# Optimization experiments

Measured on AMD Instinct MI355X. Metric: run time of the kernel, lower is better.

The kernel has to match this reference:

```python
import jax, jax.numpy as jnp
import numpy as np

B, W, T, D = 64, 32, 4096, 128

def setup_inputs() -> dict:
    key = jax.random.key(0)
    ks = jax.random.split(key, 10)
    s = 1.0 / np.sqrt(D)
    return {
        "x": jax.random.normal(ks[0], (B, W, T), dtype=jnp.float32),
        "enc_w": jax.random.uniform(ks[1], (D, W), jnp.float32, -1/np.sqrt(W), 1/np.sqrt(W)),
        "enc_b": jax.random.uniform(ks[2], (D,), jnp.float32, -1/np.sqrt(W), 1/np.sqrt(W)),
        "w_ih": jax.random.uniform(ks[3], (3 * D, D), jnp.float32, -s, s),
        "w_hh": jax.random.uniform(ks[4], (3 * D, D), jnp.float32, -s, s),
        "b_ih": jax.random.uniform(ks[5], (3 * D,), jnp.float32, -s, s),
        "b_hh": jax.random.uniform(ks[6], (3 * D,), jnp.float32, -s, s),
        "dec_w": jax.random.uniform(ks[7], (1, D), jnp.float32, -s, s),
        "dec_b": jax.random.uniform(ks[8], (1,), jnp.float32, -s, s),
        "scale": jnp.ones((1,), dtype=jnp.float32),
        "noise_eps": jax.random.normal(ks[9], (B, T), dtype=jnp.float32),
    }

def reference(x, enc_w, enc_b, w_ih, w_hh, b_ih, b_hh, dec_w, dec_b, scale, noise_eps):
    # x: [B, W, T] -> src: [T, B, W]
    src = jnp.transpose(x, (2, 0, 1))
    encoded = src @ enc_w.T + enc_b  # [T, B, D] (dropout is identity at inference)

    def gru_step(h, xt):
        gi = xt @ w_ih.T + b_ih  # [B, 3D]
        gh = h @ w_hh.T + b_hh   # [B, 3D]
        i_r, i_z, i_n = jnp.split(gi, 3, axis=-1)
        h_r, h_z, h_n = jnp.split(gh, 3, axis=-1)
        r = jax.nn.sigmoid(i_r + h_r)
        z = jax.nn.sigmoid(i_z + h_z)
        n = jnp.tanh(i_n + r * h_n)
        h_new = (1.0 - z) * n + z * h
        return h_new, h_new

    h0 = jnp.zeros_like(encoded[0])
    _, res = jax.lax.scan(gru_step, h0, encoded)  # res: [T, B, D]

    out = encoded + res
    out = (out @ dec_w.T + dec_b)[..., 0]  # [T, B]
    out = out.T                            # [B, T]
    noise = scale * noise_eps              # scale * randn_like(x[:, -1, :])
    return jax.nn.relu(out + noise)
```

## Files before the change

### kernel.cpp

```cpp
#include <hip/hip_runtime.h>

#define NB 64
#define NW 32
#define NT 4096
#define ND 128

#define GI_DW 516
#define HR_STRIDE 144

typedef __attribute__((ext_vector_type(8))) short short8;
typedef __attribute__((ext_vector_type(4))) float f32x4;

#define BAR_LGKM() asm volatile("s_waitcnt lgkmcnt(0)\n\ts_barrier" ::: "memory")

static __device__ __forceinline__ float sigm_f(float v) {
    float e = __builtin_amdgcn_exp2f(v * -1.4426950408889634f);
    return __builtin_amdgcn_rcpf(1.0f + e);
}
static __device__ __forceinline__ float tanh_f(float v) {
    float e = __builtin_amdgcn_exp2f(v * 2.8853900817779268f);
    return 1.0f - 2.0f * __builtin_amdgcn_rcpf(1.0f + e);
}
static __device__ __forceinline__ unsigned short f2bf(float f) {
    unsigned u = __float_as_uint(f);
    u += 0x7FFFu + ((u >> 16) & 1u);
    return (unsigned short)(u >> 16);
}

__global__ __launch_bounds__(256) void k_xv(
    const float* __restrict__ x, const float* __restrict__ enc_w,
    const float* __restrict__ enc_b, const float* __restrict__ dec_w,
    const float* __restrict__ dec_b, const float* __restrict__ scale,
    const float* __restrict__ noise, float* __restrict__ out)
{
    __shared__ float v_s[NW];
    __shared__ float c2_s;
    const int tid = threadIdx.x;
    if (tid < NW) {
        float s = 0.0f;
        for (int d = 0; d < ND; ++d) s = fmaf(enc_w[d * NW + tid], dec_w[d], s);
        v_s[tid] = s;
    } else if (tid == 64) {
        float s = 0.0f;
        for (int d = 0; d < ND; ++d) s = fmaf(enc_b[d], dec_w[d], s);
        c2_s = s + dec_b[0];
    }
    __syncthreads();
    const int flat = blockIdx.x * 256 + tid;
    const int b = flat >> 12;
    const int t = flat & (NT - 1);
    float acc = c2_s + scale[0] * noise[flat];
    const float* xr = x + (size_t)b * NW * NT + t;
    #pragma unroll
    for (int w = 0; w < NW; ++w) acc = fmaf(xr[(size_t)w * NT], v_s[w], acc);
    out[flat] = acc;
}

__global__ __launch_bounds__(256, 1) void k_gru(
    const float* __restrict__ x, const float* __restrict__ enc_w,
    const float* __restrict__ enc_b, const float* __restrict__ w_ih,
    const float* __restrict__ w_hh, const float* __restrict__ b_ih,
    const float* __restrict__ b_hh, const float* __restrict__ dec_w,
    float* out)
{
    __shared__ alignas(16) float gi_lds[32 * GI_DW];
    __shared__ float encb_s[ND];
    __shared__ alignas(16) unsigned short h_ring[32 * HR_STRIDE];
    __shared__ alignas(16) float xv_lds[NT];
    __shared__ alignas(16) float out_lds[NT];

    const int tid  = threadIdx.x;
    const int b    = blockIdx.x;
    const int wv   = tid >> 6;
    const int lane = tid & 63;
    const int g    = lane >> 4;
    const int c    = lane & 15;
    const int hi   = g & 1;
    const int d0   = wv * 32 + c;
    const int d1   = d0 + 16;
    const int dl   = wv * 32 + (lane & 31);

    const size_t xbase = (size_t)b * NW * NT;
    float* outb = out + (size_t)b * NT;
    float* encw_s = gi_lds;

    for (int i = tid; i < ND * NW; i += 256) encw_s[i] = enc_w[i];
    if (tid < ND) encb_s[tid] = enc_b[tid];
    for (int i = tid; i < 32 * HR_STRIDE; i += 256) h_ring[i] = 0;
    for (int i = tid; i < NT / 4; i += 256)
        ((float4*)xv_lds)[i] = ((const float4*)outb)[i];
    __syncthreads();

    short8 BR0[4], BZ0[4], BN0[4], BR1[4], BZ1[4], BN1[4];
    #pragma unroll
    for (int kt = 0; kt < 4; ++kt) {
        const float* pr0 = w_hh + (size_t)(0*ND + d0) * ND + kt*32 + g*8;
        const float* pz0 = w_hh + (size_t)(1*ND + d0) * ND + kt*32 + g*8;
        const float* pn0 = w_hh + (size_t)(2*ND + d0) * ND + kt*32 + g*8;
        const float* pr1 = w_hh + (size_t)(0*ND + d1) * ND + kt*32 + g*8;
        const float* pz1 = w_hh + (size_t)(1*ND + d1) * ND + kt*32 + g*8;
        const float* pn1 = w_hh + (size_t)(2*ND + d1) * ND + kt*32 + g*8;
        #pragma unroll
        for (int i = 0; i < 8; ++i) {
            BR0[kt][i] = (short)f2bf(pr0[i]);
            BZ0[kt][i] = (short)f2bf(pz0[i]);
            BN0[kt][i] = (short)f2bf(pn0[i]);
            BR1[kt][i] = (short)f2bf(pr1[i]);
            BZ1[kt][i] = (short)f2bf(pz1[i]);
            BN1[kt][i] = (short)f2bf(pn1[i]);
        }
    }

    short8 BD[4];
    #pragma unroll
    for (int kt = 0; kt < 4; ++kt)
        #pragma unroll
        for (int i = 0; i < 8; ++i)
            BD[kt][i] = (short)f2bf(dec_w[kt*32 + g*8 + i]);

    short8 XR0, XZ0, XN0, XR1, XZ1, XN1;
    {
        const float* rr0 = w_ih + (size_t)(0*ND + d0) * ND;
        const float* rz0 = w_ih + (size_t)(1*ND + d0) * ND;
        const float* rn0 = w_ih + (size_t)(2*ND + d0) * ND;
        const float* rr1 = w_ih + (size_t)(0*ND + d1) * ND;
        const float* rz1 = w_ih + (size_t)(1*ND + d1) * ND;
        const float* rn1 = w_ih + (size_t)(2*ND + d1) * ND;
        #pragma unroll
        for (int i = 0; i < 8; ++i) {
            int w = g*8 + i;
            float ar0 = 0.f, az0 = 0.f, an0 = 0.f, ar1 = 0.f, az1 = 0.f, an1 = 0.f;
            for (int dp = 0; dp < ND; ++dp) {
                float ew = encw_s[dp*NW + w];
                ar0 = fmaf(ew, rr0[dp], ar0);
                az0 = fmaf(ew, rz0[dp], az0);
                an0 = fmaf(ew, rn0[dp], an0);
                ar1 = fmaf(ew, rr1[dp], ar1);
                az1 = fmaf(ew, rz1[dp], az1);
                an1 = fmaf(ew, rn1[dp], an1);
            }
            XR0[i] = (short)f2bf(ar0); XZ0[i] = (short)f2bf(az0); XN0[i] = (short)f2bf(an0);
            XR1[i] = (short)f2bf(ar1); XZ1[i] = (short)f2bf(az1); XN1[i] = (short)f2bf(an1);
        }
    }

    float cR0, cZ0, cGN0, cIN0, cR1, cZ1, cGN1, cIN1;
    {
        const float* rr0 = w_ih + (size_t)(0*ND + d0) * ND;
        const float* rz0 = w_ih + (size_t)(1*ND + d0) * ND;
        const float* rn0 = w_ih + (size_t)(2*ND + d0) * ND;
        const float* rr1 = w_ih + (size_t)(0*ND + d1) * ND;
        const float* rz1 = w_ih + (size_t)(1*ND + d1) * ND;
        const float* rn1 = w_ih + (size_t)(2*ND + d1) * ND;
        float a0 = b_ih[d0], a1 = b_ih[ND+d0], a2 = b_ih[2*ND+d0];
        float e0 = b_ih[d1], e1 = b_ih[ND+d1], e2 = b_ih[2*ND+d1];
        for (int dp = 0; dp < ND; ++dp) {
            float eb = encb_s[dp];
            a0 = fmaf(eb, rr0[dp], a0);
            a1 = fmaf(eb, rz0[dp], a1);
            a2 = fmaf(eb, rn0[dp], a2);
            e0 = fmaf(eb, rr1[dp], e0);
            e1 = fmaf(eb, rz1[dp], e1);
            e2 = fmaf(eb, rn1[dp], e2);
        }
        cR0  = a0 + b_hh[d0];
        cZ0  = a1 + b_hh[ND+d0];
        cGN0 = b_hh[2*ND+d0];
        cIN0 = a2;
        cR1  = e0 + b_hh[d1];
        cZ1  = e1 + b_hh[ND+d1];
        cGN1 = b_hh[2*ND+d1];
        cIN1 = e2;
    }
    const f32x4 cRv0  = {cR0, cR0, cR0, cR0};
    const f32x4 cZv0  = {cZ0, cZ0, cZ0, cZ0};
    const f32x4 cGNv0 = {cGN0, cGN0, cGN0, cGN0};
    const f32x4 cINv0 = {cIN0, cIN0, cIN0, cIN0};
    const f32x4 cRv1  = {cR1, cR1, cR1, cR1};
    const f32x4 cZv1  = {cZ1, cZ1, cZ1, cZ1};
    const f32x4 cGNv1 = {cGN1, cGN1, cGN1, cGN1};
    const f32x4 cINv1 = {cIN1, cIN1, cIN1, cIN1};
    const f32x4 zv    = {0.f, 0.f, 0.f, 0.f};

    __syncthreads();

    float xf[8];
    #pragma unroll
    for (int q = 0; q < 8; ++q)
        xf[q] = x[xbase + (size_t)(g*8 + q) * NT + c];
    {
        short8 xA;
        #pragma unroll
        for (int i = 0; i < 8; ++i) xA[i] = (short)f2bf(xf[i]);
        f32x4 gR0 = __builtin_amdgcn_mfma_f32_16x16x32_bf16(xA, XR0, cRv0, 0, 0, 0);
        f32x4 gZ0 = __builtin_amdgcn_mfma_f32_16x16x32_bf16(xA, XZ0, cZv0, 0, 0, 0);
        f32x4 gN0 = __builtin_amdgcn_mfma_f32_16x16x32_bf16(xA, XN0, cINv0, 0, 0, 0);
        f32x4 gR1 = __builtin_amdgcn_mfma_f32_16x16x32_bf16(xA, XR1, cRv1, 0, 0, 0);
        f32x4 gZ1 = __builtin_amdgcn_mfma_f32_16x16x32_bf16(xA, XZ1, cZv1, 0, 0, 0);
        f32x4 gN1 = __builtin_amdgcn_mfma_f32_16x16x32_bf16(xA, XN1, cINv1, 0, 0, 0);
        #pragma unroll
        for (int r = 0; r < 4; ++r) {
            int ti = 4*g + r;
            f32x4 p0 = {gR0[r], gZ0[r], gN0[r], 0.f};
            f32x4 p1 = {gR1[r], gZ1[r], gN1[r], 0.f};
            *(f32x4*)(gi_lds + (size_t)ti * GI_DW + d0 * 4) = p0;
            *(f32x4*)(gi_lds + (size_t)ti * GI_DW + d1 * 4) = p1;
        }
    }
    #pragma unroll
    for (int q = 0; q < 8; ++q)
        xf[q] = x[xbase + (size_t)(g*8 + q) * NT + 16 + c];

    __syncthreads();

    float h = 0.0f;

    #pragma unroll 1
    for (int t = 0; t < NT; ++t) {
        const short8* hp = (const short8*)(h_ring + (size_t)((t + 31) & 31) * HR_STRIDE);
        const short8 HA0 = hp[0*4 + g];
        const short8 HA1 = hp[1*4 + g];
        const short8 HA2 = hp[2*4 + g];
        const short8 HA3 = hp[3*4 + g];

        const f32x4 giv = *(const f32x4*)(gi_lds + (size_t)(t & 31) * GI_DW + dl * 4);

        f32x4 aR1_0 = __builtin_amdgcn_mfma_f32_16x16x32_bf16(HA0, BR0[0], zv, 0, 0, 0);
        f32x4 aR2_0 = __builtin_amdgcn_mfma_f32_16x16x32_bf16(HA2, BR0[2], zv, 0, 0, 0);
        f32x4 aR1_1 = __builtin_amdgcn_mfma_f32_16x16x32_bf16(HA0, BR1[0], zv, 0, 0, 0);
        f32x4 aR2_1 = __builtin_amdgcn_mfma_f32_16x16x32_bf16(HA2, BR1[2], zv, 0, 0, 0);
        aR1_0 = __builtin_amdgcn_mfma_f32_16x16x32_bf16(HA1, BR0[1], aR1_0, 0, 0, 0);
        aR2_0 = __builtin_amdgcn_mfma_f32_16x16x32_bf16(HA3, BR0[3], aR2_0, 0, 0, 0);
        aR1_1 = __builtin_amdgcn_mfma_f32_16x16x32_bf16(HA1, BR1[1], aR1_1, 0, 0, 0);
        aR2_1 = __builtin_amdgcn_mfma_f32_16x16x32_bf16(HA3, BR1[3], aR2_1, 0, 0, 0);
        f32x4 aZ1_0 = __builtin_amdgcn_mfma_f32_16x16x32_bf16(HA0, BZ0[0], zv, 0, 0, 0);
        f32x4 aZ2_0 = __builtin_amdgcn_mfma_f32_16x16x32_bf16(HA2, BZ0[2], zv, 0, 0, 0);
        f32x4 aZ1_1 = __builtin_amdgcn_mfma_f32_16x16x32_bf16(HA0, BZ1[0], zv, 0, 0, 0);
        f32x4 aZ2_1 = __builtin_amdgcn_mfma_f32_16x16x32_bf16(HA2, BZ1[2], zv, 0, 0, 0);
        aZ1_0 = __builtin_amdgcn_mfma_f32_16x16x32_bf16(HA1, BZ0[1], aZ1_0, 0, 0, 0);
        aZ2_0 = __builtin_amdgcn_mfma_f32_16x16x32_bf16(HA3, BZ0[3], aZ2_0, 0, 0, 0);
        aZ1_1 = __builtin_amdgcn_mfma_f32_16x16x32_bf16(HA1, BZ1[1], aZ1_1, 0, 0, 0);
        aZ2_1 = __builtin_amdgcn_mfma_f32_16x16x32_bf16(HA3, BZ1[3], aZ2_1, 0, 0, 0);
        f32x4 aN1_0 = __builtin_amdgcn_mfma_f32_16x16x32_bf16(HA0, BN0[0], cGNv0, 0, 0, 0);
        f32x4 aN2_0 = __builtin_amdgcn_mfma_f32_16x16x32_bf16(HA2, BN0[2], zv, 0, 0, 0);
        f32x4 aN1_1 = __builtin_amdgcn_mfma_f32_16x16x32_bf16(HA0, BN1[0], cGNv1, 0, 0, 0);
        f32x4 aN2_1 = __builtin_amdgcn_mfma_f32_16x16x32_bf16(HA2, BN1[2], zv, 0, 0, 0);
        aN1_0 = __builtin_amdgcn_mfma_f32_16x16x32_bf16(HA1, BN0[1], aN1_0, 0, 0, 0);
        aN2_0 = __builtin_amdgcn_mfma_f32_16x16x32_bf16(HA3, BN0[3], aN2_0, 0, 0, 0);
        aN1_1 = __builtin_amdgcn_mfma_f32_16x16x32_bf16(HA1, BN1[1], aN1_1, 0, 0, 0);
        aN2_1 = __builtin_amdgcn_mfma_f32_16x16x32_bf16(HA3, BN1[3], aN2_1, 0, 0, 0);

        float R  = hi ? (aR1_1[0] + aR2_1[0]) : (aR1_0[0] + aR2_0[0]);
        float Z  = hi ? (aZ1_1[0] + aZ2_1[0]) : (aZ1_0[0] + aZ2_0[0]);
        float GN = hi ? (aN1_1[0] + aN2_1[0]) : (aN1_0[0] + aN2_0[0]);
        float r_ = sigm_f(R + giv[0]);
        float z_ = sigm_f(Z + giv[1]);
        float n_ = tanh_f(fmaf(r_, GN, giv[2]));
        h = fmaf(z_, h - n_, n_);
        if (lane < 32) h_ring[(size_t)(t & 31) * HR_STRIDE + dl] = f2bf(h);

        if ((t & 15) == 8) {
            const int t0n = (t & ~15) + 16;
            if (t0n < NT) {
                short8 xA;
                #pragma unroll
                for (int i = 0; i < 8; ++i) xA[i] = (short)f2bf(xf[i]);
                f32x4 gR0 = __builtin_amdgcn_mfma_f32_16x16x32_bf16(xA, XR0, cRv0, 0, 0, 0);
                f32x4 gZ0 = __builtin_amdgcn_mfma_f32_16x16x32_bf16(xA, XZ0, cZv0, 0, 0, 0);
                f32x4 gN0 = __builtin_amdgcn_mfma_f32_16x16x32_bf16(xA, XN0, cINv0, 0, 0, 0);
                f32x4 gR1 = __builtin_amdgcn_mfma_f32_16x16x32_bf16(xA, XR1, cRv1, 0, 0, 0);
                f32x4 gZ1 = __builtin_amdgcn_mfma_f32_16x16x32_bf16(xA, XZ1, cZv1, 0, 0, 0);
                f32x4 gN1 = __builtin_amdgcn_mfma_f32_16x16x32_bf16(xA, XN1, cINv1, 0, 0, 0);
                const int rb = t0n & 31;
                #pragma unroll
                for (int r = 0; r < 4; ++r) {
                    int ti = rb + 4*g + r;
                    f32x4 p0 = {gR0[r], gZ0[r], gN0[r], 0.f};
                    f32x4 p1 = {gR1[r], gZ1[r], gN1[r], 0.f};
                    *(f32x4*)(gi_lds + (size_t)ti * GI_DW + d0 * 4) = p0;
                    *(f32x4*)(gi_lds + (size_t)ti * GI_DW + d1 * 4) = p1;
                }
                const int t0p = t0n + 16;
                if (t0p < NT) {
                    #pragma unroll
                    for (int q = 0; q < 8; ++q)
                        xf[q] = x[xbase + (size_t)(g*8 + q) * NT + t0p + c];
                }
            }
        }

        if ((t & 15) == 0 && t >= 16 && wv == (((t >> 4) - 1) & 3)) {
            const short8* hq = (const short8*)(h_ring + (size_t)(((t - 16) & 31) + c) * HR_STRIDE);
            short8 AD0 = hq[0*4 + g];
            short8 AD1 = hq[1*4 + g];
            short8 AD2 = hq[2*4 + g];
            short8 AD3 = hq[3*4 + g];
            f32x4 aD1 = __builtin_amdgcn_mfma_f32_16x16x32_bf16(AD0, BD[0], zv, 0, 0, 0);
            f32x4 aD2 = __builtin_amdgcn_mfma_f32_16x16x32_bf16(AD2, BD[2], zv, 0, 0, 0);
            aD1 = __builtin_amdgcn_mfma_f32_16x16x32_bf16(AD1, BD[1], aD1, 0, 0, 0);
            aD2 = __builtin_amdgcn_mfma_f32_16x16x32_bf16(AD3, BD[3], aD2, 0, 0, 0);
            if (c == 0) {
                #pragma unroll
                for (int r = 0; r < 4; ++r)
                    out_lds[(t - 16) + 4*g + r] = aD1[r] + aD2[r];
            }
        }

        BAR_LGKM();
    }

    if (wv == 0) {
        const short8* hq = (const short8*)(h_ring + (size_t)(16 + c) * HR_STRIDE);
        short8 AD0 = hq[0*4 + g];
        short8 AD1 = hq[1*4 + g];
        short8 AD2 = hq[2*4 + g];
        short8 AD3 = hq[3*4 + g];
        f32x4 aD1 = __builtin_amdgcn_mfma_f32_16x16x32_bf16(AD0, BD[0], zv, 0, 0, 0);
        f32x4 aD2 = __builtin_amdgcn_mfma_f32_16x16x32_bf16(AD2, BD[2], zv, 0, 0, 0);
        aD1 = __builtin_amdgcn_mfma_f32_16x16x32_bf16(AD1, BD[1], aD1, 0, 0, 0);
        aD2 = __builtin_amdgcn_mfma_f32_16x16x32_bf16(AD3, BD[3], aD2, 0, 0, 0);
        if (c == 0) {
            #pragma unroll
            for (int r = 0; r < 4; ++r)
                out_lds[(NT - 16) + 4*g + r] = aD1[r] + aD2[r];
        }
    }
    __syncthreads();
    for (int i = tid; i < NT / 4; i += 256) {
        float4 o = ((const float4*)out_lds)[i];
        float4 v = ((const float4*)xv_lds)[i];
        float4 r;
        r.x = fmaxf(o.x + v.x, 0.0f);
        r.y = fmaxf(o.y + v.y, 0.0f);
        r.z = fmaxf(o.z + v.z, 0.0f);
        r.w = fmaxf(o.w + v.w, 0.0f);
        ((float4*)outb)[i] = r;
    }
}

extern "C" void kernel_launch(void* const* d_in, const int* in_sizes, int n_in,
                              void* d_out, int out_size, void* d_ws, size_t ws_size,
                              hipStream_t stream) {
    const float* x      = (const float*)d_in[0];
    const float* enc_w  = (const float*)d_in[1];
    const float* enc_b  = (const float*)d_in[2];
    const float* w_ih   = (const float*)d_in[3];
    const float* w_hh   = (const float*)d_in[4];
    const float* b_ih   = (const float*)d_in[5];
    const float* b_hh   = (const float*)d_in[6];
    const float* dec_w  = (const float*)d_in[7];
    const float* dec_b  = (const float*)d_in[8];
    const float* scale  = (const float*)d_in[9];
    const float* noise  = (const float*)d_in[10];
    float* out = (float*)d_out;

    k_xv<<<(NB * NT) / 256, 256, 0, stream>>>(x, enc_w, enc_b, dec_w, dec_b, scale, noise, out);
    k_gru<<<NB, 256, 0, stream>>>(x, enc_w, enc_b, w_ih, w_hh, b_ih, b_hh, dec_w, out);
}
```

Baseline: 1.764 ms.

## Specialize waves: recurrence waves separate from input-projection and decoder waves

```diff
diff --git a/kernel.cpp b/kernel.cpp
--- a/kernel.cpp
+++ b/kernel.cpp
@@ -25,6 +25,11 @@
     unsigned u = __float_as_uint(f);
     u += 0x7FFFu + ((u >> 16) & 1u);
     return (unsigned short)(u >> 16);
+}
+static __device__ __forceinline__ unsigned cvt_pk_bf16(float a, float b) {
+    unsigned r;
+    asm("v_cvt_pk_bf16_f32 %0, %1, %2" : "=v"(r) : "v"(a), "v"(b));
+    return r;
 }
 
 __global__ __launch_bounds__(256) void k_xv(
@@ -56,7 +61,7 @@
     out[flat] = acc;
 }
 
-__global__ __launch_bounds__(256, 1) void k_gru(
+__global__ __launch_bounds__(512, 1) void k_gru(
     const float* __restrict__ x, const float* __restrict__ enc_w,
     const float* __restrict__ enc_b, const float* __restrict__ w_ih,
     const float* __restrict__ w_hh, const float* __restrict__ b_ih,
@@ -76,50 +81,55 @@
     const int g    = lane >> 4;
     const int c    = lane & 15;
     const int hi   = g & 1;
-    const int d0   = wv * 32 + c;
+    const int p    = wv - 4;
+    const int dg   = (wv < 4 ? wv : p);
+    const int d0   = dg * 32 + c;
     const int d1   = d0 + 16;
-    const int dl   = wv * 32 + (lane & 31);
+    const int dl   = dg * 32 + (lane & 31);
 
     const size_t xbase = (size_t)b * NW * NT;
     float* outb = out + (size_t)b * NT;
     float* encw_s = gi_lds;
 
-    for (int i = tid; i < ND * NW; i += 256) encw_s[i] = enc_w[i];
+    for (int i = tid; i < ND * NW; i += 512) encw_s[i] = enc_w[i];
     if (tid < ND) encb_s[tid] = enc_b[tid];
-    for (int i = tid; i < 32 * HR_STRIDE; i += 256) h_ring[i] = 0;
-    for (int i = tid; i < NT / 4; i += 256)
+    for (int i = tid; i < 32 * HR_STRIDE; i += 512) h_ring[i] = 0;
+    for (int i = tid; i < NT / 4; i += 512) {
         ((float4*)xv_lds)[i] = ((const float4*)outb)[i];
+        ((float4*)out_lds)[i] = make_float4(0.f, 0.f, 0.f, 0.f);
+    }
     __syncthreads();
 
     short8 BR0[4], BZ0[4], BN0[4], BR1[4], BZ1[4], BN1[4];
-    #pragma unroll
-    for (int kt = 0; kt < 4; ++kt) {
-        const float* pr0 = w_hh + (size_t)(0*ND + d0) * ND + kt*32 + g*8;
-        const float* pz0 = w_hh + (size_t)(1*ND + d0) * ND + kt*32 + g*8;
-        const float* pn0 = w_hh + (size_t)(2*ND + d0) * ND + kt*32 + g*8;
-        const float* pr1 = w_hh + (size_t)(0*ND + d1) * ND + kt*32 + g*8;
-        const float* pz1 = w_hh + (size_t)(1*ND + d1) * ND + kt*32 + g*8;
-        const float* pn1 = w_hh + (size_t)(2*ND + d1) * ND + kt*32 + g*8;
-        #pragma unroll
-        for (int i = 0; i < 8; ++i) {
-            BR0[kt][i] = (short)f2bf(pr0[i]);
-            BZ0[kt][i] = (short)f2bf(pz0[i]);
-            BN0[kt][i] = (short)f2bf(pn0[i]);
-            BR1[kt][i] = (short)f2bf(pr1[i]);
-            BZ1[kt][i] = (short)f2bf(pz1[i]);
-            BN1[kt][i] = (short)f2bf(pn1[i]);
-        }
-    }
-
-    short8 BD[4];
-    #pragma unroll
-    for (int kt = 0; kt < 4; ++kt)
-        #pragma unroll
-        for (int i = 0; i < 8; ++i)
-            BD[kt][i] = (short)f2bf(dec_w[kt*32 + g*8 + i]);
-
-    short8 XR0, XZ0, XN0, XR1, XZ1, XN1;
-    {
+    f32x4 cGNv0 = {0.f, 0.f, 0.f, 0.f}, cGNv1 = {0.f, 0.f, 0.f, 0.f};
+    short8 XR0, XZ0, XN0, XR1, XZ1, XN1, BDd;
+    f32x4 cRv0, cZv0, cINv0, cRv1, cZv1, cINv1;
+    float xf[8];
+    const f32x4 zv = {0.f, 0.f, 0.f, 0.f};
+
+    if (wv < 4) {
+        #pragma unroll
+        for (int kt = 0; kt < 4; ++kt) {
+            const float* pr0 = w_hh + (size_t)(0*ND + d0) * ND + kt*32 + g*8;
+            const float* pz0 = w_hh + (size_t)(1*ND + d0) * ND + kt*32 + g*8;
+            const float* pn0 = w_hh + (size_t)(2*ND + d0) * ND + kt*32 + g*8;
+            const float* pr1 = w_hh + (size_t)(0*ND + d1) * ND + kt*32 + g*8;
+            const float* pz1 = w_hh + (size_t)(1*ND + d1) * ND + kt*32 + g*8;
+            const float* pn1 = w_hh + (size_t)(2*ND + d1) * ND + kt*32 + g*8;
+            #pragma unroll
+            for (int i = 0; i < 8; ++i) {
+                BR0[kt][i] = (short)f2bf(pr0[i]);
+                BZ0[kt][i] = (short)f2bf(pz0[i]);
+                BN0[kt][i] = (short)f2bf(pn0[i]);
+                BR1[kt][i] = (short)f2bf(pr1[i]);
+                BZ1[kt][i] = (short)f2bf(pz1[i]);
+                BN1[kt][i] = (short)f2bf(pn1[i]);
+            }
+        }
+        float g0 = b_hh[2*ND + d0], g1 = b_hh[2*ND + d1];
+        cGNv0 = (f32x4){g0, g0, g0, g0};
+        cGNv1 = (f32x4){g1, g1, g1, g1};
+    } else {
         const float* rr0 = w_ih + (size_t)(0*ND + d0) * ND;
         const float* rz0 = w_ih + (size_t)(1*ND + d0) * ND;
         const float* rn0 = w_ih + (size_t)(2*ND + d0) * ND;
@@ -142,16 +152,6 @@
             XR0[i] = (short)f2bf(ar0); XZ0[i] = (short)f2bf(az0); XN0[i] = (short)f2bf(an0);
             XR1[i] = (short)f2bf(ar1); XZ1[i] = (short)f2bf(az1); XN1[i] = (short)f2bf(an1);
         }
-    }
-
-    float cR0, cZ0, cGN0, cIN0, cR1, cZ1, cGN1, cIN1;
-    {
-        const float* rr0 = w_ih + (size_t)(0*ND + d0) * ND;
-        const float* rz0 = w_ih + (size_t)(1*ND + d0) * ND;
-        const float* rn0 = w_ih + (size_t)(2*ND + d0) * ND;
-        const float* rr1 = w_ih + (size_t)(0*ND + d1) * ND;
-        const float* rz1 = w_ih + (size_t)(1*ND + d1) * ND;
-        const float* rn1 = w_ih + (size_t)(2*ND + d1) * ND;
         float a0 = b_ih[d0], a1 = b_ih[ND+d0], a2 = b_ih[2*ND+d0];
         float e0 = b_ih[d1], e1 = b_ih[ND+d1], e2 = b_ih[2*ND+d1];
         for (int dp = 0; dp < ND; ++dp) {
@@ -163,32 +163,24 @@
             e1 = fmaf(eb, rz1[dp], e1);
             e2 = fmaf(eb, rn1[dp], e2);
         }
-        cR0  = a0 + b_hh[d0];
-        cZ0  = a1 + b_hh[ND+d0];
-        cGN0 = b_hh[2*ND+d0];
-        cIN0 = a2;
-        cR1  = e0 + b_hh[d1];
-        cZ1  = e1 + b_hh[ND+d1];
-        cGN1 = b_hh[2*ND+d1];
-        cIN1 = e2;
-    }
-    const f32x4 cRv0  = {cR0, cR0, cR0, cR0};
-    const f32x4 cZv0  = {cZ0, cZ0, cZ0, cZ0};
-    const f32x4 cGNv0 = {cGN0, cGN0, cGN0, cGN0};
-    const f32x4 cINv0 = {cIN0, cIN0, cIN0, cIN0};
-    const f32x4 cRv1  = {cR1, cR1, cR1, cR1};
-    const f32x4 cZv1  = {cZ1, cZ1, cZ1, cZ1};
-    const f32x4 cGNv1 = {cGN1, cGN1, cGN1, cGN1};
-    const f32x4 cINv1 = {cIN1, cIN1, cIN1, cIN1};
-    const f32x4 zv    = {0.f, 0.f, 0.f, 0.f};
-
-    __syncthreads();
-
-    float xf[8];
-    #pragma unroll
-    for (int q = 0; q < 8; ++q)
-        xf[q] = x[xbase + (size_t)(g*8 + q) * NT + c];
-    {
+        float cR0 = a0 + b_hh[d0],  cZ0 = a1 + b_hh[ND+d0];
+        float cR1 = e0 + b_hh[d1],  cZ1 = e1 + b_hh[ND+d1];
+        cRv0 = (f32x4){cR0, cR0, cR0, cR0};
+        cZv0 = (f32x4){cZ0, cZ0, cZ0, cZ0};
+        cINv0 = (f32x4){a2, a2, a2, a2};
+        cRv1 = (f32x4){cR1, cR1, cR1, cR1};
+        cZv1 = (f32x4){cZ1, cZ1, cZ1, cZ1};
+        cINv1 = (f32x4){e2, e2, e2, e2};
+        #pragma unroll
+        for (int i = 0; i < 8; ++i) BDd[i] = (short)f2bf(dec_w[p*32 + g*8 + i]);
+    }
+
+    __syncthreads();
+
+    if (wv >= 4) {
+        #pragma unroll
+        for (int q = 0; q < 8; ++q)
+            xf[q] = x[xbase + (size_t)(g*8 + q) * NT + c];
         short8 xA;
         #pragma unroll
         for (int i = 0; i < 8; ++i) xA[i] = (short)f2bf(xf[i]);
@@ -206,119 +198,124 @@
             *(f32x4*)(gi_lds + (size_t)ti * GI_DW + d0 * 4) = p0;
             *(f32x4*)(gi_lds + (size_t)ti * GI_DW + d1 * 4) = p1;
         }
-    }
-    #pragma unroll
-    for (int q = 0; q < 8; ++q)
-        xf[q] = x[xbase + (size_t)(g*8 + q) * NT + 16 + c];
+        #pragma unroll
+        for (int q = 0; q < 8; ++q)
+            xf[q] = x[xbase + (size_t)(g*8 + q) * NT + 16 + c];
+    }
 
     __syncthreads();
 
     float h = 0.0f;
+    f32x4 giv = *(const f32x4*)(gi_lds + dl * 4);
 
     #pragma unroll 1
     for (int t = 0; t < NT; ++t) {
-        const short8* hp = (const short8*)(h_ring + (size_t)((t + 31) & 31) * HR_STRIDE);
-        const short8 HA0 = hp[0*4 + g];
-        const short8 HA1 = hp[1*4 + g];
-        const short8 HA2 = hp[2*4 + g];
-        const short8 HA3 = hp[3*4 + g];
-
-        const f32x4 giv = *(const f32x4*)(gi_lds + (size_t)(t & 31) * GI_DW + dl * 4);
-
-        f32x4 aR1_0 = __builtin_amdgcn_mfma_f32_16x16x32_bf16(HA0, BR0[0], zv, 0, 0, 0);
-        f32x4 aR2_0 = __builtin_amdgcn_mfma_f32_16x16x32_bf16(HA2, BR0[2], zv, 0, 0, 0);
-        f32x4 aR1_1 = __builtin_amdgcn_mfma_f32_16x16x32_bf16(HA0, BR1[0], zv, 0, 0, 0);
-        f32x4 aR2_1 = __builtin_amdgcn_mfma_f32_16x16x32_bf16(HA2, BR1[2], zv, 0, 0, 0);
-        aR1_0 = __builtin_amdgcn_mfma_f32_16x16x32_bf16(HA1, BR0[1], aR1_0, 0, 0, 0);
-        aR2_0 = __builtin_amdgcn_mfma_f32_16x16x32_bf16(HA3, BR0[3], aR2_0, 0, 0, 0);
-        aR1_1 = __builtin_amdgcn_mfma_f32_16x16x32_bf16(HA1, BR1[1], aR1_1, 0, 0, 0);
-        aR2_1 = __builtin_amdgcn_mfma_f32_16x16x32_bf16(HA3, BR1[3], aR2_1, 0, 0, 0);
-        f32x4 aZ1_0 = __builtin_amdgcn_mfma_f32_16x16x32_bf16(HA0, BZ0[0], zv, 0, 0, 0);
-        f32x4 aZ2_0 = __builtin_amdgcn_mfma_f32_16x16x32_bf16(HA2, BZ0[2], zv, 0, 0, 0);
-        f32x4 aZ1_1 = __builtin_amdgcn_mfma_f32_16x16x32_bf16(HA0, BZ1[0], zv, 0, 0, 0);
-        f32x4 aZ2_1 = __builtin_amdgcn_mfma_f32_16x16x32_bf16(HA2, BZ1[2], zv, 0, 0, 0);
-        aZ1_0 = __builtin_amdgcn_mfma_f32_16x16x32_bf16(HA1, BZ0[1], aZ1_0, 0, 0, 0);
-        aZ2_0 = __builtin_amdgcn_mfma_f32_16x16x32_bf16(HA3, BZ0[3], aZ2_0, 0, 0, 0);
-        aZ1_1 = __builtin_amdgcn_mfma_f32_16x16x32_bf16(HA1, BZ1[1], aZ1_1, 0, 0, 0);
-        aZ2_1 = __builtin_amdgcn_mfma_f32_16x16x32_bf16(HA3, BZ1[3], aZ2_1, 0, 0, 0);
-        f32x4 aN1_0 = __builtin_amdgcn_mfma_f32_16x16x32_bf16(HA0, BN0[0], cGNv0, 0, 0, 0);
-        f32x4 aN2_0 = __builtin_amdgcn_mfma_f32_16x16x32_bf16(HA2, BN0[2], zv, 0, 0, 0);
-        f32x4 aN1_1 = __builtin_amdgcn_mfma_f32_16x16x32_bf16(HA0, BN1[0], cGNv1, 0, 0, 0);
-        f32x4 aN2_1 = __builtin_amdgcn_mfma_f32_16x16x32_bf16(HA2, BN1[2], zv, 0, 0, 0);
-        aN1_0 = __builtin_amdgcn_mfma_f32_16x16x32_bf16(HA1, BN0[1], aN1_0, 0, 0, 0);
-        aN2_0 = __builtin_amdgcn_mfma_f32_16x16x32_bf16(HA3, BN0[3], aN2_0, 0, 0, 0);
-        aN1_1 = __builtin_amdgcn_mfma_f32_16x16x32_bf16(HA1, BN1[1], aN1_1, 0, 0, 0);
-        aN2_1 = __builtin_amdgcn_mfma_f32_16x16x32_bf16(HA3, BN1[3], aN2_1, 0, 0, 0);
-
-        float R  = hi ? (aR1_1[0] + aR2_1[0]) : (aR1_0[0] + aR2_0[0]);
-        float Z  = hi ? (aZ1_1[0] + aZ2_1[0]) : (aZ1_0[0] + aZ2_0[0]);
-        float GN = hi ? (aN1_1[0] + aN2_1[0]) : (aN1_0[0] + aN2_0[0]);
-        float r_ = sigm_f(R + giv[0]);
-        float z_ = sigm_f(Z + giv[1]);
-        float n_ = tanh_f(fmaf(r_, GN, giv[2]));
-        h = fmaf(z_, h - n_, n_);
-        if (lane < 32) h_ring[(size_t)(t & 31) * HR_STRIDE + dl] = f2bf(h);
-
-        if ((t & 15) == 8) {
-            const int t0n = (t & ~15) + 16;
-            if (t0n < NT) {
-                short8 xA;
-                #pragma unroll
-                for (int i = 0; i < 8; ++i) xA[i] = (short)f2bf(xf[i]);
-                f32x4 gR0 = __builtin_amdgcn_mfma_f32_16x16x32_bf16(xA, XR0, cRv0, 0, 0, 0);
-                f32x4 gZ0 = __builtin_amdgcn_mfma_f32_16x16x32_bf16(xA, XZ0, cZv0, 0, 0, 0);
-                f32x4 gN0 = __builtin_amdgcn_mfma_f32_16x16x32_bf16(xA, XN0, cINv0, 0, 0, 0);
-                f32x4 gR1 = __builtin_amdgcn_mfma_f32_16x16x32_bf16(xA, XR1, cRv1, 0, 0, 0);
-                f32x4 gZ1 = __builtin_amdgcn_mfma_f32_16x16x32_bf16(xA, XZ1, cZv1, 0, 0, 0);
-                f32x4 gN1 = __builtin_amdgcn_mfma_f32_16x16x32_bf16(xA, XN1, cINv1, 0, 0, 0);
-                const int rb = t0n & 31;
-                #pragma unroll
-                for (int r = 0; r < 4; ++r) {
-                    int ti = rb + 4*g + r;
-                    f32x4 p0 = {gR0[r], gZ0[r], gN0[r], 0.f};
-                    f32x4 p1 = {gR1[r], gZ1[r], gN1[r], 0.f};
-                    *(f32x4*)(gi_lds + (size_t)ti * GI_DW + d0 * 4) = p0;
-                    *(f32x4*)(gi_lds + (size_t)ti * GI_DW + d1 * 4) = p1;
-                }
-                const int t0p = t0n + 16;
-                if (t0p < NT) {
+        if (wv < 4) {
+            const short8* hp = (const short8*)(h_ring + (size_t)((t + 31) & 31) * HR_STRIDE);
+            const short8 HA0 = hp[0*4 + g];
+            const short8 HA1 = hp[1*4 + g];
+            const short8 HA2 = hp[2*4 + g];
+            const short8 HA3 = hp[3*4 + g];
+            const f32x4 gi_next = *(const f32x4*)(gi_lds + (size_t)((t + 1) & 31) * GI_DW + dl * 4);
+
+            f32x4 aR1_0 = __builtin_amdgcn_mfma_f32_16x16x32_bf16(HA0, BR0[0], zv, 0, 0, 0);
+            f32x4 aR2_0 = __builtin_amdgcn_mfma_f32_16x16x32_bf16(HA2, BR0[2], zv, 0, 0, 0);
+            f32x4 aR1_1 = __builtin_amdgcn_mfma_f32_16x16x32_bf16(HA0, BR1[0], zv, 0, 0, 0);
+            f32x4 aR2_1 = __builtin_amdgcn_mfma_f32_16x16x32_bf16(HA2, BR1[2], zv, 0, 0, 0);
+            aR1_0 = __builtin_amdgcn_mfma_f32_16x16x32_bf16(HA1, BR0[1], aR1_0, 0, 0, 0);
+            aR2_0 = __builtin_amdgcn_mfma_f32_16x16x32_bf16(HA3, BR0[3], aR2_0, 0, 0, 0);
+            aR1_1 = __builtin_amdgcn_mfma_f32_16x16x32_bf16(HA1, BR1[1], aR1_1, 0, 0, 0);
+            aR2_1 = __builtin_amdgcn_mfma_f32_16x16x32_bf16(HA3, BR1[3], aR2_1, 0, 0, 0);
+            f32x4 aN1_0 = __builtin_amdgcn_mfma_f32_16x16x32_bf16(HA0, BN0[0], cGNv0, 0, 0, 0);
+            f32x4 aN2_0 = __builtin_amdgcn_mfma_f32_16x16x32_bf16(HA2, BN0[2], zv, 0, 0, 0);
+            f32x4 aN1_1 = __builtin_amdgcn_mfma_f32_16x16x32_bf16(HA0, BN1[0], cGNv1, 0, 0, 0);
+            f32x4 aN2_1 = __builtin_amdgcn_mfma_f32_16x16x32_bf16(HA2, BN1[2], zv, 0, 0, 0);
+            aN1_0 = __builtin_amdgcn_mfma_f32_16x16x32_bf16(HA1, BN0[1], aN1_0, 0, 0, 0);
+            aN2_0 = __builtin_amdgcn_mfma_f32_16x16x32_bf16(HA3, BN0[3], aN2_0, 0, 0, 0);
+            aN1_1 = __builtin_amdgcn_mfma_f32_16x16x32_bf16(HA1, BN1[1], aN1_1, 0, 0, 0);
+            aN2_1 = __builtin_amdgcn_mfma_f32_16x16x32_bf16(HA3, BN1[3], aN2_1, 0, 0, 0);
+
+            float Rs = (hi ? aR1_1[0] : aR1_0[0]) + (hi ? aR2_1[0] : aR2_0[0]);
+            float r_ = sigm_f(Rs + giv[0]);
+
+            f32x4 aZ1_0 = __builtin_amdgcn_mfma_f32_16x16x32_bf16(HA0, BZ0[0], zv, 0, 0, 0);
+            f32x4 aZ2_0 = __builtin_amdgcn_mfma_f32_16x16x32_bf16(HA2, BZ0[2], zv, 0, 0, 0);
+            f32x4 aZ1_1 = __builtin_amdgcn_mfma_f32_16x16x32_bf16(HA0, BZ1[0], zv, 0, 0, 0);
+            f32x4 aZ2_1 = __builtin_amdgcn_mfma_f32_16x16x32_bf16(HA2, BZ1[2], zv, 0, 0, 0);
+            aZ1_0 = __builtin_amdgcn_mfma_f32_16x16x32_bf16(HA1, BZ0[1], aZ1_0, 0, 0, 0);
+            aZ2_0 = __builtin_amdgcn_mfma_f32_16x16x32_bf16(HA3, BZ0[3], aZ2_0, 0, 0, 0);
+            aZ1_1 = __builtin_amdgcn_mfma_f32_16x16x32_bf16(HA1, BZ1[1], aZ1_1, 0, 0, 0);
+            aZ2_1 = __builtin_amdgcn_mfma_f32_16x16x32_bf16(HA3, BZ1[3], aZ2_1, 0, 0, 0);
+
+            float GNs = (hi ? aN1_1[0] : aN1_0[0]) + (hi ? aN2_1[0] : aN2_0[0]);
+            float n_ = tanh_f(fmaf(r_, GNs, giv[2]));
+            float Zs = (hi ? aZ1_1[0] : aZ1_0[0]) + (hi ? aZ2_1[0] : aZ2_0[0]);
+            float z_ = sigm_f(Zs + giv[1]);
+            h = fmaf(z_, h - n_, n_);
+            unsigned hpk = cvt_pk_bf16(h, h);
+            if (lane < 32) h_ring[(size_t)(t & 31) * HR_STRIDE + dl] = (unsigned short)hpk;
+            giv = gi_next;
+        } else {
+            if ((t & 15) == 8) {
+                const int t0n = (t & ~15) + 16;
+                if (t0n < NT) {
+                    short8 xA;
                     #pragma unroll
-                    for (int q = 0; q < 8; ++q)
-                        xf[q] = x[xbase + (size_t)(g*8 + q) * NT + t0p + c];
+                    for (int i = 0; i < 8; ++i) xA[i] = (short)f2bf(xf[i]);
+                    f32x4 gR0 = __builtin_amdgcn_mfma_f32_16x16x32_bf16(xA, XR0, cRv0, 0, 0, 0);
+                    f32x4 gZ0 = __builtin_amdgcn_mfma_f32_16x16x32_bf16(xA, XZ0, cZv0, 0, 0, 0);
+                    f32x4 gN0 = __builtin_amdgcn_mfma_f32_16x16x32_bf16(xA, XN0, cINv0, 0, 0, 0);
+                    f32x4 gR1 = __builtin_amdgcn_mfma_f32_16x16x32_bf16(xA, XR1, cRv1, 0, 0, 0);
+                    f32x4 gZ1 = __builtin_amdgcn_mfma_f32_16x16x32_bf16(xA, XZ1, cZv1, 0, 0, 0);
+                    f32x4 gN1 = __builtin_amdgcn_mfma_f32_16x16x32_bf16(xA, XN1, cINv1, 0, 0, 0);
+                    const int rb = t0n & 31;
+                    #pragma unroll
+                    for (int r = 0; r < 4; ++r) {
+                        int ti = rb + 4*g + r;
+                        f32x4 p0 = {gR0[r], gZ0[r], gN0[r], 0.f};
+                        f32x4 p1 = {gR1[r], gZ1[r], gN1[r], 0.f};
+                        *(f32x4*)(gi_lds + (size_t)ti * GI_DW + d0 * 4) = p0;
+                        *(f32x4*)(gi_lds + (size_t)ti * GI_DW + d1 * 4) = p1;
+                    }
+                    const int t0p = t0n + 16;
+                    if (t0p < NT) {
+                        #pragma unroll
+                        for (int q = 0; q < 8; ++q)
+                            xf[q] = x[xbase + (size_t)(g*8 + q) * NT + t0p + c];
+                    }
                 }
             }
-        }
-
-        if ((t & 15) == 0 && t >= 16 && wv == (((t >> 4) - 1) & 3)) {
-            const short8* hq = (const short8*)(h_ring + (size_t)(((t - 16) & 31) + c) * HR_STRIDE);
-            short8 AD0 = hq[0*4 + g];
-            short8 AD1 = hq[1*4 + g];
-            short8 AD2 = hq[2*4 + g];
-            short8 AD3 = hq[3*4 + g];
-            f32x4 aD1 = __builtin_amdgcn_mfma_f32_16x16x32_bf16(AD0, BD[0], zv, 0, 0, 0);
-            f32x4 aD2 = __builtin_amdgcn_mfma_f32_16x16x32_bf16(AD2, BD[2], zv, 0, 0, 0);
-            aD1 = __builtin_amdgcn_mfma_f32_16x16x32_bf16(AD1, BD[1], aD1, 0, 0, 0);
-            aD2 = __builtin_amdgcn_mfma_f32_16x16x32_bf16(AD3, BD[3], aD2, 0, 0, 0);
-            if (c == 0) {
-                #pragma unroll
-                for (int r = 0; r < 4; ++r)
-                    out_lds[(t - 16) + 4*g + r] = aD1[r] + aD2[r];
+            if ((t & 15) == (p * 4 + 2) && t >= 16) {
+                const int t0w = (t & ~15) - 16;
+                const short8* hq = (const short8*)(h_ring + (size_t)((t0w & 31) + c) * HR_STRIDE);
+                short8 AD = hq[p*4 + g];
+                f32x4 aD = __builtin_amdgcn_mfma_f32_16x16x32_bf16(AD, BDd, zv, 0, 0, 0);
+                if (c == 0) {
+                    #pragma unroll
+                    for (int r = 0; r < 4; ++r)
+                        out_lds[t0w + 4*g + r] += aD[r];
+                }
             }
         }
-
         BAR_LGKM();
     }
 
-    if (wv == 0) {
+    if (wv == 4) {
+        short8 BDk[4];
+        #pragma unroll
+        for (int kt = 0; kt < 4; ++kt)
+            #pragma unroll
+            for (int i = 0; i < 8; ++i)
+                BDk[kt][i] = (short)f2bf(dec_w[kt*32 + g*8 + i]);
         const short8* hq = (const short8*)(h_ring + (size_t)(16 + c) * HR_STRIDE);
         short8 AD0 = hq[0*4 + g];
         short8 AD1 = hq[1*4 + g];
         short8 AD2 = hq[2*4 + g];
         short8 AD3 = hq[3*4 + g];
-        f32x4 aD1 = __builtin_amdgcn_mfma_f32_16x16x32_bf16(AD0, BD[0], zv, 0, 0, 0);
-        f32x4 aD2 = __builtin_amdgcn_mfma_f32_16x16x32_bf16(AD2, BD[2], zv, 0, 0, 0);
-        aD1 = __builtin_amdgcn_mfma_f32_16x16x32_bf16(AD1, BD[1], aD1, 0, 0, 0);
-        aD2 = __builtin_amdgcn_mfma_f32_16x16x32_bf16(AD3, BD[3], aD2, 0, 0, 0);
+        f32x4 aD1 = __builtin_amdgcn_mfma_f32_16x16x32_bf16(AD0, BDk[0], zv, 0, 0, 0);
+        f32x4 aD2 = __builtin_amdgcn_mfma_f32_16x16x32_bf16(AD2, BDk[2], zv, 0, 0, 0);
+        aD1 = __builtin_amdgcn_mfma_f32_16x16x32_bf16(AD1, BDk[1], aD1, 0, 0, 0);
+        aD2 = __builtin_amdgcn_mfma_f32_16x16x32_bf16(AD3, BDk[3], aD2, 0, 0, 0);
         if (c == 0) {
             #pragma unroll
             for (int r = 0; r < 4; ++r)
@@ -326,7 +323,7 @@
         }
     }
     __syncthreads();
-    for (int i = tid; i < NT / 4; i += 256) {
+    for (int i = tid; i < NT / 4; i += 512) {
         float4 o = ((const float4*)out_lds)[i];
         float4 v = ((const float4*)xv_lds)[i];
         float4 r;
@@ -355,5 +352,5 @@
     float* out = (float*)d_out;
 
     k_xv<<<(NB * NT) / 256, 256, 0, stream>>>(x, enc_w, enc_b, dec_w, dec_b, scale, noise, out);
-    k_gru<<<NB, 256, 0, stream>>>(x, enc_w, enc_b, w_ih, w_hh, b_ih, b_hh, dec_w, out);
-}
+    k_gru<<<NB, 512, 0, stream>>>(x, enc_w, enc_b, w_ih, w_hh, b_ih, b_hh, dec_w, out);
+}
```

After: 1.745 ms. Within noise of the previous version (-1.1%).
